# Kernel optimization log

Hardware: AMD Instinct MI355X
Metric: run time of the kernel (lower is better)

The kernel has to match this reference:

```python
import jax, jax.numpy as jnp
import numpy as np

C = 128
HEAD_CHANNEL = 32
NUM_HEAD = C // HEAD_CHANNEL
SCALE = HEAD_CHANNEL ** 0.5
EPS = 1e-5


def _layernorm(x, g, b):
    mu = jnp.mean(x, axis=-1, keepdims=True)
    var = jnp.mean((x - mu) ** 2, axis=-1, keepdims=True)
    return (x - mu) * jax.lax.rsqrt(var + EPS) * g + b


def _proj(x, g, b, w1, b1, w2, b2):
    # LayerNorm -> Linear(C,2C) -> LeakyReLU(0.01) -> Linear(2C,C); dropout=0 (identity)
    h = jax.nn.leaky_relu(_layernorm(x, g, b) @ w1 + b1, negative_slope=0.01)
    return h @ w2 + b2


def _mlp(x, w1, b1, w2, b2):
    h = jax.nn.leaky_relu(x @ w1 + b1, negative_slope=0.01)
    return h @ w2 + b2


def setup_inputs() -> dict:
    key = jax.random.key(0)
    ks = jax.random.split(key, 32)
    s = 1.0 / np.sqrt(C)
    s2 = 1.0 / np.sqrt(2 * C)
    d = {}
    d["q"] = jax.random.normal(ks[0], (2, C, 64, 64), jnp.float32)
    d["k"] = jax.random.normal(ks[1], (2, C, 64, 64), jnp.float32)
    d["v"] = jax.random.normal(ks[2], (2, C, 64, 64), jnp.float32)
    i = 3
    for p in ("q", "k", "v"):
        d[f"ln_{p}_g"] = jnp.ones((C,), jnp.float32)
        d[f"ln_{p}_b"] = jnp.zeros((C,), jnp.float32)
        d[f"w{p}1"] = jax.random.uniform(ks[i], (C, 2 * C), jnp.float32, -s, s); i += 1
        d[f"b{p}1"] = jnp.zeros((2 * C,), jnp.float32)
        d[f"w{p}2"] = jax.random.uniform(ks[i], (2 * C, C), jnp.float32, -s2, s2); i += 1
        d[f"b{p}2"] = jnp.zeros((C,), jnp.float32)
    for m in ("m1", "m2"):
        d[f"{m}_w1"] = jax.random.uniform(ks[i], (C, 2 * C), jnp.float32, -s, s); i += 1
        d[f"{m}_b1"] = jnp.zeros((2 * C,), jnp.float32)
        d[f"{m}_w2"] = jax.random.uniform(ks[i], (2 * C, C), jnp.float32, -s2, s2); i += 1
        d[f"{m}_b2"] = jnp.zeros((C,), jnp.float32)
    return d


def reference(q, k, v,
              ln_q_g, ln_q_b, wq1, bq1, wq2, bq2,
              ln_k_g, ln_k_b, wk1, bk1, wk2, bk2,
              ln_v_g, ln_v_b, wv1, bv1, wv2, bv2,
              m1_w1, m1_b1, m1_w2, m1_b2,
              m2_w1, m2_b1, m2_w2, m2_b2):
    B, Cc, H, W = q.shape
    S = H * W
    # [B,C,H,W] -> [B,S,C] token layout
    qt = q.transpose(0, 2, 3, 1).reshape(B, S, Cc)
    kt = k.transpose(0, 2, 3, 1).reshape(B, S, Cc)
    vt = v.transpose(0, 2, 3, 1).reshape(B, S, Cc)
    qp = _proj(qt, ln_q_g, ln_q_b, wq1, bq1, wq2, bq2)
    kp = _proj(kt, ln_k_g, ln_k_b, wk1, bk1, wk2, bk2)
    vp = _proj(vt, ln_v_g, ln_v_b, wv1, bv1, wv2, bv2)  # v_attn_1
    qh = qp.reshape(B, S, NUM_HEAD, HEAD_CHANNEL)
    kh = kp.reshape(B, S, NUM_HEAD, HEAD_CHANNEL)
    vh = vp.reshape(B, S, NUM_HEAD, HEAD_CHANNEL)
    attn = jax.nn.softmax(jnp.einsum('bqhd,bkhd->bhqk', qh, kh) / SCALE, axis=-1)
    x = jnp.einsum('bhqk,bkhd->bqhd', attn, vh).reshape(B, S, Cc)
    rs1 = vp + _mlp(x, m1_w1, m1_b1, m1_w2, m1_b2)
    rs2 = rs1 + _mlp(rs1, m2_w1, m2_b1, m2_w2, m2_b2)
    # back to [B,C,H,W]
    return rs2.reshape(B, H, W, Cc).transpose(0, 3, 1, 2)
```

## Files before the change

kernel.cpp:

```cpp
#include <hip/hip_runtime.h>
#include <hip/hip_bf16.h>

typedef __bf16 bf16_t;
typedef __bf16 bf16x4 __attribute__((ext_vector_type(4)));
typedef __bf16 bf16x8 __attribute__((ext_vector_type(8)));
typedef float f32x4 __attribute__((ext_vector_type(4)));
typedef float f32x16 __attribute__((ext_vector_type(16)));


static constexpr size_t WS_WPK   = 0;
static constexpr size_t WS_PP    = 655360;
static constexpr size_t WS_VT    = WS_PP + 3ull*2097152;
static constexpr size_t WS_OPART = WS_VT + 2097152;
static constexpr size_t WS_LPART = WS_OPART + 16777216;

struct WPtrs { const float* w1[5]; const float* w2[5]; };

__global__ __launch_bounds__(256) void prep_weights(WPtrs wp, bf16_t* __restrict__ dst) {
    __shared__ float ts[64][65];
    int bx = blockIdx.x;
    int p = bx >> 4;
    int t = bx & 15;
    const float* src; int sld, dld, r0, c0; bf16_t* d;
    if (t < 8) {
        src = wp.w1[p]; sld = 256; dld = 128;
        r0 = (t >> 2) * 64; c0 = (t & 3) * 64;
        d = dst + p * 65536;
    } else {
        int tt = t - 8;
        src = wp.w2[p]; sld = 128; dld = 256;
        r0 = (tt >> 1) * 64; c0 = (tt & 1) * 64;
        d = dst + p * 65536 + 32768;
    }
    for (int i = threadIdx.x; i < 4096; i += 256) {
        int r = i >> 6, c = i & 63;
        ts[r][c] = src[(r0 + r) * sld + c0 + c];
    }
    __syncthreads();
    for (int i = threadIdx.x; i < 4096; i += 256) {
        int c = i >> 6, r = i & 63;
        d[(c0 + c) * dld + (r0 + r)] = (bf16_t)ts[r][c];
    }
}

struct ProjArgs {
    const float* src[3]; const float* g[3]; const float* bb[3];
    const float* B1[3]; const float* B2[3];
    bf16_t* OUT[3]; bf16_t* VTOUT;
};

__global__ __launch_bounds__(256) void projln_kernel(ProjArgs a, const bf16_t* __restrict__ wpk) {
    __shared__ float xs[16][132];
    __shared__ bf16_t al[16][136];
    __shared__ bf16_t hl[16][264];
    int z = blockIdx.y;
    int m0 = blockIdx.x * 16;
    int b = m0 >> 12, s0 = m0 & 4095;
    int tx = threadIdx.x;
    int w = tx >> 6;
    int lane = tx & 63;
    int quad = lane >> 4;
    int l15 = lane & 15;

    const float* src = a.src[z];
    for (int idx = tx; idx < 2048; idx += 256) {
        int c = idx >> 4, tt = idx & 15;
        xs[tt][c] = src[(b * 128 + c) * 4096 + s0 + tt];
    }
    __syncthreads();

    {
        int t = tx >> 4, j = tx & 15;
        float sum = 0.f, sq = 0.f;
#pragma unroll
        for (int k = 0; k < 8; ++k) { float v = xs[t][j + 16 * k]; sum += v; sq += v * v; }
        sum += __shfl_xor(sum, 1); sq += __shfl_xor(sq, 1);
        sum += __shfl_xor(sum, 2); sq += __shfl_xor(sq, 2);
        sum += __shfl_xor(sum, 4); sq += __shfl_xor(sq, 4);
        sum += __shfl_xor(sum, 8); sq += __shfl_xor(sq, 8);
        float mu = sum * (1.0f / 128.0f);
        float var = sq * (1.0f / 128.0f) - mu * mu;
        float rs = rsqrtf(var + 1e-5f);
        const float* g = a.g[z];
        const float* bb = a.bb[z];
#pragma unroll
        for (int k = 0; k < 8; ++k) {
            int c = j + 16 * k;
            al[t][c] = (bf16_t)((xs[t][c] - mu) * rs * g[c] + bb[c]);
        }
    }
    __syncthreads();

    const bf16_t* w1t = wpk + (size_t)z * 65536;
    const bf16_t* w2t = w1t + 32768;
    bf16x8 af[4];
#pragma unroll
    for (int kt = 0; kt < 4; ++kt) af[kt] = *(const bf16x8*)(&al[l15][kt * 32 + quad * 8]);

#pragma unroll
    for (int sub = 0; sub < 4; ++sub) {
        int n = w * 64 + sub * 16 + l15;
        const bf16_t* wrow = w1t + (size_t)n * 128 + quad * 8;
        f32x4 acc = {0.f, 0.f, 0.f, 0.f};
#pragma unroll
        for (int kt = 0; kt < 4; ++kt) {
            bf16x8 bfrag = *(const bf16x8*)(wrow + kt * 32);
            acc = __builtin_amdgcn_mfma_f32_16x16x32_bf16(af[kt], bfrag, acc, 0, 0, 0);
        }
        float bn = a.B1[z][n];
#pragma unroll
        for (int r = 0; r < 4; ++r) {
            float v = acc[r] + bn;
            v = v > 0.f ? v : 0.01f * v;
            hl[quad * 4 + r][n] = (bf16_t)v;
        }
    }
    __syncthreads();

    bf16x8 hf[8];
#pragma unroll
    for (int kt = 0; kt < 8; ++kt)
        hf[kt] = *(const bf16x8*)(&hl[l15][kt * 32 + quad * 8]);

#pragma unroll
    for (int sub = 0; sub < 2; ++sub) {
        int n = w * 32 + sub * 16 + l15;
        const bf16_t* wrow = w2t + (size_t)n * 256 + quad * 8;
        f32x4 acc = {0.f, 0.f, 0.f, 0.f};
#pragma unroll
        for (int kt = 0; kt < 8; ++kt) {
            bf16x8 bfrag = *(const bf16x8*)(wrow + kt * 32);
            acc = __builtin_amdgcn_mfma_f32_16x16x32_bf16(hf[kt], bfrag, acc, 0, 0, 0);
        }
        float bn = a.B2[z][n];
        float vals[4];
#pragma unroll
        for (int r = 0; r < 4; ++r) vals[r] = acc[r] + bn;
#pragma unroll
        for (int r = 0; r < 4; ++r)
            a.OUT[z][(size_t)(m0 + quad * 4 + r) * 128 + n] = (bf16_t)vals[r];
        if (z == 2) {
            int bh = b * 4 + (n >> 5), d = n & 31;
            bf16x4 tv = {(bf16_t)vals[0], (bf16_t)vals[1], (bf16_t)vals[2], (bf16_t)vals[3]};
            *(bf16x4*)(a.VTOUT + ((size_t)(bh * 32 + d)) * 4096 + s0 + quad * 4) = tv;
        }
    }
}

__global__ __launch_bounds__(256, 4) void attn_kernel(const bf16_t* __restrict__ qp,
                                                      const bf16_t* __restrict__ kp,
                                                      const bf16_t* __restrict__ vt,
                                                      bf16_t* __restrict__ opart,
                                                      float* __restrict__ lpart) {
    int lid = blockIdx.x;
    int bh = lid & 7;
    int r = lid >> 3;
    int split = r & 7;
    int qb = r >> 3;
    int w = threadIdx.x >> 6;
    int lane = threadIdx.x & 63;
    int l31 = lane & 31;
    int h5 = lane >> 5;
    int b = bh >> 2, h = bh & 3;
    int q0 = qb * 256 + w * 64;

    constexpr float kScale = 0.17677669529663687f * 1.4426950408889634f;

    bf16x8 qf[2][2];
#pragma unroll
    for (int s = 0; s < 2; ++s) {
        const bf16_t* qrow = qp + ((size_t)(b * 4096 + q0 + s * 32 + l31)) * 128 + h * 32 + h5 * 8;
        bf16x8 q0r = *(const bf16x8*)(qrow);
        bf16x8 q1r = *(const bf16x8*)(qrow + 16);
#pragma unroll
        for (int j = 0; j < 8; ++j) {
            qf[s][0][j] = (bf16_t)((float)q0r[j] * kScale);
            qf[s][1][j] = (bf16_t)((float)q1r[j] * kScale);
        }
    }

    bf16x8 a_up, a_lo;
    {
        bf16_t one = (bf16_t)1.0f, zer = (bf16_t)0.0f;
#pragma unroll
        for (int j = 0; j < 8; ++j) { a_up[j] = (l31 < 16) ? one : zer; a_lo[j] = (l31 < 16) ? zer : one; }
    }

    int key_m = (l31 & ~12) | ((l31 & 4) << 1) | ((l31 & 8) >> 1);
    const bf16_t* kbase = kp + ((size_t)(b * 4096) + key_m) * 128 + h * 32 + h5 * 8;
    const bf16_t* vbase = vt + ((size_t)(bh * 32) + l31) * 4096 + h5 * 8;

    f32x16 acca = {0.f,0.f,0.f,0.f,0.f,0.f,0.f,0.f,0.f,0.f,0.f,0.f,0.f,0.f,0.f,0.f};
    f32x16 accb = acca, lacc = acca;
    f32x16 zero16 = acca;

    int kt0 = split * 16;
    const bf16_t* kpt = kbase + (size_t)kt0 * 4096;
    const bf16_t* vpt = vbase + kt0 * 32;
    bf16x8 kf0 = *(const bf16x8*)(kpt);
    bf16x8 kf1 = *(const bf16x8*)(kpt + 16);
    bf16x8 vf0 = *(const bf16x8*)(vpt);
    bf16x8 vf1 = *(const bf16x8*)(vpt + 16);

    for (int it = 0; it < 16; ++it) {
        const bf16_t* nkpt = kpt + (it < 15 ? 4096 : 0);
        const bf16_t* nvpt = vpt + (it < 15 ? 32 : 0);
        bf16x8 nk0 = *(const bf16x8*)(nkpt);
        bf16x8 nk1 = *(const bf16x8*)(nkpt + 16);
        bf16x8 nv0 = *(const bf16x8*)(nvpt);
        bf16x8 nv1 = *(const bf16x8*)(nvpt + 16);

        f32x16 sca = __builtin_amdgcn_mfma_f32_32x32x16_bf16(kf0, qf[0][0], zero16, 0, 0, 0);
        sca = __builtin_amdgcn_mfma_f32_32x32x16_bf16(kf1, qf[0][1], sca, 0, 0, 0);
        f32x16 scb = __builtin_amdgcn_mfma_f32_32x32x16_bf16(kf0, qf[1][0], zero16, 0, 0, 0);
        scb = __builtin_amdgcn_mfma_f32_32x32x16_bf16(kf1, qf[1][1], scb, 0, 0, 0);

        bf16x8 pfa0, pfa1, pfb0, pfb1;
#pragma unroll
        for (int j = 0; j < 8; ++j) {
            pfa0[j] = (bf16_t)__builtin_amdgcn_exp2f(sca[j]);
            pfa1[j] = (bf16_t)__builtin_amdgcn_exp2f(sca[8 + j]);
            pfb0[j] = (bf16_t)__builtin_amdgcn_exp2f(scb[j]);
            pfb1[j] = (bf16_t)__builtin_amdgcn_exp2f(scb[8 + j]);
        }

        lacc = __builtin_amdgcn_mfma_f32_32x32x16_bf16(a_up, pfa0, lacc, 0, 0, 0);
        lacc = __builtin_amdgcn_mfma_f32_32x32x16_bf16(a_up, pfa1, lacc, 0, 0, 0);
        lacc = __builtin_amdgcn_mfma_f32_32x32x16_bf16(a_lo, pfb0, lacc, 0, 0, 0);
        lacc = __builtin_amdgcn_mfma_f32_32x32x16_bf16(a_lo, pfb1, lacc, 0, 0, 0);

        acca = __builtin_amdgcn_mfma_f32_32x32x16_bf16(vf0, pfa0, acca, 0, 0, 0);
        acca = __builtin_amdgcn_mfma_f32_32x32x16_bf16(vf1, pfa1, acca, 0, 0, 0);
        accb = __builtin_amdgcn_mfma_f32_32x32x16_bf16(vf0, pfb0, accb, 0, 0, 0);
        accb = __builtin_amdgcn_mfma_f32_32x32x16_bf16(vf1, pfb1, accb, 0, 0, 0);

        kf0 = nk0; kf1 = nk1; vf0 = nv0; vf1 = nv1;
        kpt = nkpt; vpt = nvpt;
    }

    size_t obase0 = ((size_t)(bh * 8 + split) * 4096 + q0 + l31) * 32;
#pragma unroll
    for (int g = 0; g < 4; ++g) {
        bf16x4 ov = {(bf16_t)acca[4*g], (bf16_t)acca[4*g+1], (bf16_t)acca[4*g+2], (bf16_t)acca[4*g+3]};
        *(bf16x4*)(opart + obase0 + 8 * g + 4 * h5) = ov;
    }
    size_t obase1 = obase0 + 32ull * 32;
#pragma unroll
    for (int g = 0; g < 4; ++g) {
        bf16x4 ov = {(bf16_t)accb[4*g], (bf16_t)accb[4*g+1], (bf16_t)accb[4*g+2], (bf16_t)accb[4*g+3]};
        *(bf16x4*)(opart + obase1 + 8 * g + 4 * h5) = ov;
    }
    lpart[(bh * 8 + split) * 4096 + q0 + h5 * 32 + l31] = h5 ? lacc[8] : lacc[0];
}

__global__ __launch_bounds__(256) void mlpf_kernel(const bf16_t* __restrict__ opart,
                                                   const float* __restrict__ lpart,
                                                   const bf16_t* __restrict__ wpk,
                                                   const float* __restrict__ b1a,
                                                   const float* __restrict__ b2a,
                                                   const float* __restrict__ b1b,
                                                   const float* __restrict__ b2b,
                                                   const bf16_t* __restrict__ vp,
                                                   float* __restrict__ out) {
    __shared__ bf16_t al[16][136];
    __shared__ bf16_t al2[16][136];
    __shared__ bf16_t hl[16][264];
    int w = threadIdx.x >> 6;
    int lane = threadIdx.x & 63;
    int quad = lane >> 4;
    int l15 = lane & 15;
    int m0 = blockIdx.x * 16;
    int bb = m0 >> 12, s0 = m0 & 4095;

    const bf16_t* w1ta = wpk + 3ull * 65536;
    const bf16_t* w2ta = w1ta + 32768;
    const bf16_t* w1tb = wpk + 4ull * 65536;
    const bf16_t* w2tb = w1tb + 32768;

    {
        int t = threadIdx.x >> 4;
        int cg = threadIdx.x & 15;
        int m = m0 + t;
        int qq = m & 4095;
        int h = cg >> 2, d0 = (cg & 3) * 8;
        int bh = bb * 4 + h;
        float accv[8] = {0.f, 0.f, 0.f, 0.f, 0.f, 0.f, 0.f, 0.f};
        float l = 0.f;
#pragma unroll
        for (int s = 0; s < 8; ++s) {
            const bf16_t* op = opart + ((size_t)((bh * 8 + s) * 4096) + qq) * 32 + d0;
            bf16x8 o8 = *(const bf16x8*)op;
#pragma unroll
            for (int j = 0; j < 8; ++j) accv[j] += (float)o8[j];
            l += lpart[(bh * 8 + s) * 4096 + qq];
        }
        float invl = 1.0f / l;
        bf16x8 a8;
#pragma unroll
        for (int j = 0; j < 8; ++j) a8[j] = (bf16_t)(accv[j] * invl);
        *(bf16x8*)(&al[t][cg * 8]) = a8;
    }
    __syncthreads();

    bf16x8 af[4];
#pragma unroll
    for (int kt = 0; kt < 4; ++kt) af[kt] = *(const bf16x8*)(&al[l15][kt * 32 + quad * 8]);
#pragma unroll
    for (int sub = 0; sub < 4; ++sub) {
        int n = w * 64 + sub * 16 + l15;
        const bf16_t* wrow = w1ta + (size_t)n * 128 + quad * 8;
        f32x4 acc = {0.f, 0.f, 0.f, 0.f};
#pragma unroll
        for (int kt = 0; kt < 4; ++kt) {
            bf16x8 bfrag = *(const bf16x8*)(wrow + kt * 32);
            acc = __builtin_amdgcn_mfma_f32_16x16x32_bf16(af[kt], bfrag, acc, 0, 0, 0);
        }
        float bn = b1a[n];
#pragma unroll
        for (int r = 0; r < 4; ++r) {
            float v = acc[r] + bn;
            v = v > 0.f ? v : 0.01f * v;
            hl[quad * 4 + r][n] = (bf16_t)v;
        }
    }
    __syncthreads();

    {
        bf16x8 hf[8];
#pragma unroll
        for (int kt = 0; kt < 8; ++kt)
            hf[kt] = *(const bf16x8*)(&hl[l15][kt * 32 + quad * 8]);
#pragma unroll
        for (int sub = 0; sub < 2; ++sub) {
            int n = w * 32 + sub * 16 + l15;
            const bf16_t* wrow = w2ta + (size_t)n * 256 + quad * 8;
            f32x4 acc = {0.f, 0.f, 0.f, 0.f};
#pragma unroll
            for (int kt = 0; kt < 8; ++kt) {
                bf16x8 bfrag = *(const bf16x8*)(wrow + kt * 32);
                acc = __builtin_amdgcn_mfma_f32_16x16x32_bf16(hf[kt], bfrag, acc, 0, 0, 0);
            }
            float bn = b2a[n];
#pragma unroll
            for (int r = 0; r < 4; ++r) {
                int m = m0 + quad * 4 + r;
                float v = acc[r] + bn + (float)vp[(size_t)m * 128 + n];
                al2[quad * 4 + r][n] = (bf16_t)v;
            }
        }
    }
    __syncthreads();

    bf16x8 af2[4];
#pragma unroll
    for (int kt = 0; kt < 4; ++kt) af2[kt] = *(const bf16x8*)(&al2[l15][kt * 32 + quad * 8]);
#pragma unroll
    for (int sub = 0; sub < 4; ++sub) {
        int n = w * 64 + sub * 16 + l15;
        const bf16_t* wrow = w1tb + (size_t)n * 128 + quad * 8;
        f32x4 acc = {0.f, 0.f, 0.f, 0.f};
#pragma unroll
        for (int kt = 0; kt < 4; ++kt) {
            bf16x8 bfrag = *(const bf16x8*)(wrow + kt * 32);
            acc = __builtin_amdgcn_mfma_f32_16x16x32_bf16(af2[kt], bfrag, acc, 0, 0, 0);
        }
        float bn = b1b[n];
#pragma unroll
        for (int r = 0; r < 4; ++r) {
            float v = acc[r] + bn;
            v = v > 0.f ? v : 0.01f * v;
            hl[quad * 4 + r][n] = (bf16_t)v;
        }
    }
    __syncthreads();

    {
        bf16x8 hf[8];
#pragma unroll
        for (int kt = 0; kt < 8; ++kt)
            hf[kt] = *(const bf16x8*)(&hl[l15][kt * 32 + quad * 8]);
#pragma unroll
        for (int sub = 0; sub < 2; ++sub) {
            int n = w * 32 + sub * 16 + l15;
            const bf16_t* wrow = w2tb + (size_t)n * 256 + quad * 8;
            f32x4 acc = {0.f, 0.f, 0.f, 0.f};
#pragma unroll
            for (int kt = 0; kt < 8; ++kt) {
                bf16x8 bfrag = *(const bf16x8*)(wrow + kt * 32);
                acc = __builtin_amdgcn_mfma_f32_16x16x32_bf16(hf[kt], bfrag, acc, 0, 0, 0);
            }
            float bn = b2b[n];
            f32x4 ov;
#pragma unroll
            for (int r = 0; r < 4; ++r)
                ov[r] = acc[r] + bn + (float)al2[quad * 4 + r][n];
            *(f32x4*)(out + ((size_t)(bb * 128 + n)) * 4096 + s0 + quad * 4) = ov;
        }
    }
}

extern "C" void kernel_launch(void* const* d_in, const int* in_sizes, int n_in,
                              void* d_out, int out_size, void* d_ws, size_t ws_size,
                              hipStream_t stream) {
    const float* q = (const float*)d_in[0];
    const float* k = (const float*)d_in[1];
    const float* v = (const float*)d_in[2];
    const float* ln_g[3] = {(const float*)d_in[3], (const float*)d_in[9], (const float*)d_in[15]};
    const float* ln_b[3] = {(const float*)d_in[4], (const float*)d_in[10], (const float*)d_in[16]};
    const float* w1[5] = {(const float*)d_in[5], (const float*)d_in[11], (const float*)d_in[17],
                          (const float*)d_in[21], (const float*)d_in[25]};
    const float* b1[5] = {(const float*)d_in[6], (const float*)d_in[12], (const float*)d_in[18],
                          (const float*)d_in[22], (const float*)d_in[26]};
    const float* w2[5] = {(const float*)d_in[7], (const float*)d_in[13], (const float*)d_in[19],
                          (const float*)d_in[23], (const float*)d_in[27]};
    const float* b2[5] = {(const float*)d_in[8], (const float*)d_in[14], (const float*)d_in[20],
                          (const float*)d_in[24], (const float*)d_in[28]};
    float* out = (float*)d_out;

    char* ws = (char*)d_ws;
    bf16_t* wpk = (bf16_t*)(ws + WS_WPK);
    bf16_t* pp  = (bf16_t*)(ws + WS_PP);
    bf16_t* vtb = (bf16_t*)(ws + WS_VT);
    bf16_t* opart = (bf16_t*)(ws + WS_OPART);
    float* lpart = (float*)(ws + WS_LPART);

    WPtrs wp;
    for (int p = 0; p < 5; ++p) { wp.w1[p] = w1[p]; wp.w2[p] = w2[p]; }
    prep_weights<<<80, 256, 0, stream>>>(wp, wpk);

    ProjArgs pa;
    pa.src[0] = q; pa.src[1] = k; pa.src[2] = v;
    for (int i = 0; i < 3; ++i) {
        pa.g[i] = ln_g[i]; pa.bb[i] = ln_b[i];
        pa.B1[i] = b1[i]; pa.B2[i] = b2[i];
        pa.OUT[i] = pp + (size_t)i * 1048576;
    }
    pa.VTOUT = vtb;
    projln_kernel<<<dim3(512, 3), 256, 0, stream>>>(pa, wpk);

    attn_kernel<<<1024, 256, 0, stream>>>(pp, pp + 1048576, vtb, opart, lpart);

    mlpf_kernel<<<512, 256, 0, stream>>>(opart, lpart, wpk,
                                         b1[3], b2[3], b1[4], b2[4],
                                         pp + 2ull * 1048576, out);
}
```

Baseline: 207.5 us.

## Halve attention key splits and software-pipeline QK with PV across iterations

Reduces the key-dimension split from 8 to 4, so each attention block handles 32 key tiles and the grid shrinks to 512 blocks. This halves the partial-output buffer and the reduction work in the MLP kernel. The loop is restructured so the next tile's QK^T MFMAs are issued after the current tile's exp and PV MFMAs, overlapping the exp latency with matrix work. Launch bounds are relaxed to 2 blocks per SIMD to allow more registers, at the cost of occupancy and fewer blocks to fill the GPU.

```diff
diff --git a/kernel.cpp b/kernel.cpp
--- a/kernel.cpp
+++ b/kernel.cpp
@@ -12,7 +12,7 @@
 static constexpr size_t WS_PP    = 655360;
 static constexpr size_t WS_VT    = WS_PP + 3ull*2097152;
 static constexpr size_t WS_OPART = WS_VT + 2097152;
-static constexpr size_t WS_LPART = WS_OPART + 16777216;
+static constexpr size_t WS_LPART = WS_OPART + 8388608;
 
 struct WPtrs { const float* w1[5]; const float* w2[5]; };
 
@@ -147,7 +147,7 @@
     }
 }
 
-__global__ __launch_bounds__(256, 4) void attn_kernel(const bf16_t* __restrict__ qp,
+__global__ __launch_bounds__(256, 2) void attn_kernel(const bf16_t* __restrict__ qp,
                                                       const bf16_t* __restrict__ kp,
                                                       const bf16_t* __restrict__ vt,
                                                       bf16_t* __restrict__ opart,
@@ -155,8 +155,8 @@
     int lid = blockIdx.x;
     int bh = lid & 7;
     int r = lid >> 3;
-    int split = r & 7;
-    int qb = r >> 3;
+    int split = r & 3;
+    int qb = r >> 2;
     int w = threadIdx.x >> 6;
     int lane = threadIdx.x & 63;
     int l31 = lane & 31;
@@ -187,33 +187,34 @@
     }
 
     int key_m = (l31 & ~12) | ((l31 & 4) << 1) | ((l31 & 8) >> 1);
-    const bf16_t* kbase = kp + ((size_t)(b * 4096) + key_m) * 128 + h * 32 + h5 * 8;
-    const bf16_t* vbase = vt + ((size_t)(bh * 32) + l31) * 4096 + h5 * 8;
+    const bf16_t* kbase = kp + ((size_t)(b * 4096) + split * 1024 + key_m) * 128 + h * 32 + h5 * 8;
+    const bf16_t* vbase = vt + ((size_t)(bh * 32) + l31) * 4096 + split * 1024 + h5 * 8;
 
     f32x16 acca = {0.f,0.f,0.f,0.f,0.f,0.f,0.f,0.f,0.f,0.f,0.f,0.f,0.f,0.f,0.f,0.f};
     f32x16 accb = acca, lacc = acca;
     f32x16 zero16 = acca;
 
-    int kt0 = split * 16;
-    const bf16_t* kpt = kbase + (size_t)kt0 * 4096;
-    const bf16_t* vpt = vbase + kt0 * 32;
-    bf16x8 kf0 = *(const bf16x8*)(kpt);
-    bf16x8 kf1 = *(const bf16x8*)(kpt + 16);
-    bf16x8 vf0 = *(const bf16x8*)(vpt);
-    bf16x8 vf1 = *(const bf16x8*)(vpt + 16);
-
-    for (int it = 0; it < 16; ++it) {
-        const bf16_t* nkpt = kpt + (it < 15 ? 4096 : 0);
-        const bf16_t* nvpt = vpt + (it < 15 ? 32 : 0);
-        bf16x8 nk0 = *(const bf16x8*)(nkpt);
-        bf16x8 nk1 = *(const bf16x8*)(nkpt + 16);
-        bf16x8 nv0 = *(const bf16x8*)(nvpt);
-        bf16x8 nv1 = *(const bf16x8*)(nvpt + 16);
-
-        f32x16 sca = __builtin_amdgcn_mfma_f32_32x32x16_bf16(kf0, qf[0][0], zero16, 0, 0, 0);
-        sca = __builtin_amdgcn_mfma_f32_32x32x16_bf16(kf1, qf[0][1], sca, 0, 0, 0);
-        f32x16 scb = __builtin_amdgcn_mfma_f32_32x32x16_bf16(kf0, qf[1][0], zero16, 0, 0, 0);
-        scb = __builtin_amdgcn_mfma_f32_32x32x16_bf16(kf1, qf[1][1], scb, 0, 0, 0);
+    bf16x8 kcur0 = *(const bf16x8*)(kbase);
+    bf16x8 kcur1 = *(const bf16x8*)(kbase + 16);
+    bf16x8 vuse0 = *(const bf16x8*)(vbase);
+    bf16x8 vuse1 = *(const bf16x8*)(vbase + 16);
+
+    f32x16 sca = __builtin_amdgcn_mfma_f32_32x32x16_bf16(kcur0, qf[0][0], zero16, 0, 0, 0);
+    sca = __builtin_amdgcn_mfma_f32_32x32x16_bf16(kcur1, qf[0][1], sca, 0, 0, 0);
+    f32x16 scb = __builtin_amdgcn_mfma_f32_32x32x16_bf16(kcur0, qf[1][0], zero16, 0, 0, 0);
+    scb = __builtin_amdgcn_mfma_f32_32x32x16_bf16(kcur1, qf[1][1], scb, 0, 0, 0);
+
+    bf16x8 kfB0 = *(const bf16x8*)(kbase + 4096);
+    bf16x8 kfB1 = *(const bf16x8*)(kbase + 4096 + 16);
+    bf16x8 vfB0 = *(const bf16x8*)(vbase + 32);
+    bf16x8 vfB1 = *(const bf16x8*)(vbase + 32 + 16);
+
+    for (int it = 1; it < 32; ++it) {
+        int nt = (it < 31) ? it + 1 : 31;
+        bf16x8 nk0 = *(const bf16x8*)(kbase + (size_t)nt * 4096);
+        bf16x8 nk1 = *(const bf16x8*)(kbase + (size_t)nt * 4096 + 16);
+        bf16x8 nv0 = *(const bf16x8*)(vbase + nt * 32);
+        bf16x8 nv1 = *(const bf16x8*)(vbase + nt * 32 + 16);
 
         bf16x8 pfa0, pfa1, pfb0, pfb1;
 #pragma unroll
@@ -223,22 +224,44 @@
             pfb0[j] = (bf16_t)__builtin_amdgcn_exp2f(scb[j]);
             pfb1[j] = (bf16_t)__builtin_amdgcn_exp2f(scb[8 + j]);
         }
-
         lacc = __builtin_amdgcn_mfma_f32_32x32x16_bf16(a_up, pfa0, lacc, 0, 0, 0);
         lacc = __builtin_amdgcn_mfma_f32_32x32x16_bf16(a_up, pfa1, lacc, 0, 0, 0);
         lacc = __builtin_amdgcn_mfma_f32_32x32x16_bf16(a_lo, pfb0, lacc, 0, 0, 0);
         lacc = __builtin_amdgcn_mfma_f32_32x32x16_bf16(a_lo, pfb1, lacc, 0, 0, 0);
-
-        acca = __builtin_amdgcn_mfma_f32_32x32x16_bf16(vf0, pfa0, acca, 0, 0, 0);
-        acca = __builtin_amdgcn_mfma_f32_32x32x16_bf16(vf1, pfa1, acca, 0, 0, 0);
-        accb = __builtin_amdgcn_mfma_f32_32x32x16_bf16(vf0, pfb0, accb, 0, 0, 0);
-        accb = __builtin_amdgcn_mfma_f32_32x32x16_bf16(vf1, pfb1, accb, 0, 0, 0);
-
-        kf0 = nk0; kf1 = nk1; vf0 = nv0; vf1 = nv1;
-        kpt = nkpt; vpt = nvpt;
-    }
-
-    size_t obase0 = ((size_t)(bh * 8 + split) * 4096 + q0 + l31) * 32;
+        acca = __builtin_amdgcn_mfma_f32_32x32x16_bf16(vuse0, pfa0, acca, 0, 0, 0);
+        acca = __builtin_amdgcn_mfma_f32_32x32x16_bf16(vuse1, pfa1, acca, 0, 0, 0);
+        accb = __builtin_amdgcn_mfma_f32_32x32x16_bf16(vuse0, pfb0, accb, 0, 0, 0);
+        accb = __builtin_amdgcn_mfma_f32_32x32x16_bf16(vuse1, pfb1, accb, 0, 0, 0);
+
+        sca = __builtin_amdgcn_mfma_f32_32x32x16_bf16(kfB0, qf[0][0], zero16, 0, 0, 0);
+        sca = __builtin_amdgcn_mfma_f32_32x32x16_bf16(kfB1, qf[0][1], sca, 0, 0, 0);
+        scb = __builtin_amdgcn_mfma_f32_32x32x16_bf16(kfB0, qf[1][0], zero16, 0, 0, 0);
+        scb = __builtin_amdgcn_mfma_f32_32x32x16_bf16(kfB1, qf[1][1], scb, 0, 0, 0);
+
+        vuse0 = vfB0; vuse1 = vfB1;
+        kfB0 = nk0; kfB1 = nk1; vfB0 = nv0; vfB1 = nv1;
+    }
+
+    {
+        bf16x8 pfa0, pfa1, pfb0, pfb1;
+#pragma unroll
+        for (int j = 0; j < 8; ++j) {
+            pfa0[j] = (bf16_t)__builtin_amdgcn_exp2f(sca[j]);
+            pfa1[j] = (bf16_t)__builtin_amdgcn_exp2f(sca[8 + j]);
+            pfb0[j] = (bf16_t)__builtin_amdgcn_exp2f(scb[j]);
+            pfb1[j] = (bf16_t)__builtin_amdgcn_exp2f(scb[8 + j]);
+        }
+        lacc = __builtin_amdgcn_mfma_f32_32x32x16_bf16(a_up, pfa0, lacc, 0, 0, 0);
+        lacc = __builtin_amdgcn_mfma_f32_32x32x16_bf16(a_up, pfa1, lacc, 0, 0, 0);
+        lacc = __builtin_amdgcn_mfma_f32_32x32x16_bf16(a_lo, pfb0, lacc, 0, 0, 0);
+        lacc = __builtin_amdgcn_mfma_f32_32x32x16_bf16(a_lo, pfb1, lacc, 0, 0, 0);
+        acca = __builtin_amdgcn_mfma_f32_32x32x16_bf16(vuse0, pfa0, acca, 0, 0, 0);
+        acca = __builtin_amdgcn_mfma_f32_32x32x16_bf16(vuse1, pfa1, acca, 0, 0, 0);
+        accb = __builtin_amdgcn_mfma_f32_32x32x16_bf16(vuse0, pfb0, accb, 0, 0, 0);
+        accb = __builtin_amdgcn_mfma_f32_32x32x16_bf16(vuse1, pfb1, accb, 0, 0, 0);
+    }
+
+    size_t obase0 = ((size_t)(bh * 4 + split) * 4096 + q0 + l31) * 32;
 #pragma unroll
     for (int g = 0; g < 4; ++g) {
         bf16x4 ov = {(bf16_t)acca[4*g], (bf16_t)acca[4*g+1], (bf16_t)acca[4*g+2], (bf16_t)acca[4*g+3]};
@@ -250,7 +273,7 @@
         bf16x4 ov = {(bf16_t)accb[4*g], (bf16_t)accb[4*g+1], (bf16_t)accb[4*g+2], (bf16_t)accb[4*g+3]};
         *(bf16x4*)(opart + obase1 + 8 * g + 4 * h5) = ov;
     }
-    lpart[(bh * 8 + split) * 4096 + q0 + h5 * 32 + l31] = h5 ? lacc[8] : lacc[0];
+    lpart[(bh * 4 + split) * 4096 + q0 + h5 * 32 + l31] = h5 ? lacc[8] : lacc[0];
 }
 
 __global__ __launch_bounds__(256) void mlpf_kernel(const bf16_t* __restrict__ opart,
@@ -287,12 +310,12 @@
         float accv[8] = {0.f, 0.f, 0.f, 0.f, 0.f, 0.f, 0.f, 0.f};
         float l = 0.f;
 #pragma unroll
-        for (int s = 0; s < 8; ++s) {
-            const bf16_t* op = opart + ((size_t)((bh * 8 + s) * 4096) + qq) * 32 + d0;
+        for (int s = 0; s < 4; ++s) {
+            const bf16_t* op = opart + ((size_t)((bh * 4 + s) * 4096) + qq) * 32 + d0;
             bf16x8 o8 = *(const bf16x8*)op;
 #pragma unroll
             for (int j = 0; j < 8; ++j) accv[j] += (float)o8[j];
-            l += lpart[(bh * 8 + s) * 4096 + qq];
+            l += lpart[(bh * 4 + s) * 4096 + qq];
         }
         float invl = 1.0f / l;
         bf16x8 a8;
@@ -438,7 +461,7 @@
     pa.VTOUT = vtb;
     projln_kernel<<<dim3(512, 3), 256, 0, stream>>>(pa, wpk);
 
-    attn_kernel<<<1024, 256, 0, stream>>>(pp, pp + 1048576, vtb, opart, lpart);
+    attn_kernel<<<512, 256, 0, stream>>>(pp, pp + 1048576, vtb, opart, lpart);
 
     mlpf_kernel<<<512, 256, 0, stream>>>(opart, lpart, wpk,
                                          b1[3], b2[3], b1[4], b2[4],
```

Result: faster. 201.6 us (-2.8%).

## Fuse attention with both MLPs, reducing key-split partials in shared memory

Applied to the files above, without the earlier changes.

Merges the attention kernel and the MLP kernel into one launch. Each 512-thread block owns 32 query tokens across all 4 heads, with the key range split in two halves across waves. The partial outputs and row sums are combined in LDS rather than written to and re-read from global opart/lpart buffers. This removes the global partial round trip and one launch, and software-pipelines the QK^T MFMA one tile ahead of the PV step. The trade-off is a grid of only 256 blocks, each doing a 64-iteration serial key loop, which may under-fill the GPU compared with the previous 1024-block, 8-way key split.

```diff
diff --git a/kernel.cpp b/kernel.cpp
--- a/kernel.cpp
+++ b/kernel.cpp
@@ -8,11 +8,9 @@
 typedef float f32x16 __attribute__((ext_vector_type(16)));
 
 
-static constexpr size_t WS_WPK   = 0;
-static constexpr size_t WS_PP    = 655360;
-static constexpr size_t WS_VT    = WS_PP + 3ull*2097152;
-static constexpr size_t WS_OPART = WS_VT + 2097152;
-static constexpr size_t WS_LPART = WS_OPART + 16777216;
+static constexpr size_t WS_WPK = 0;
+static constexpr size_t WS_PP  = 655360;
+static constexpr size_t WS_VT  = WS_PP + 3ull*2097152;
 
 struct WPtrs { const float* w1[5]; const float* w2[5]; };
 
@@ -147,254 +145,255 @@
     }
 }
 
-__global__ __launch_bounds__(256, 4) void attn_kernel(const bf16_t* __restrict__ qp,
-                                                      const bf16_t* __restrict__ kp,
-                                                      const bf16_t* __restrict__ vt,
-                                                      bf16_t* __restrict__ opart,
-                                                      float* __restrict__ lpart) {
-    int lid = blockIdx.x;
-    int bh = lid & 7;
-    int r = lid >> 3;
-    int split = r & 7;
-    int qb = r >> 3;
-    int w = threadIdx.x >> 6;
-    int lane = threadIdx.x & 63;
+__global__ __launch_bounds__(512, 2) void attn_mlp_kernel(const bf16_t* __restrict__ qp,
+                                                          const bf16_t* __restrict__ kp,
+                                                          const bf16_t* __restrict__ vt,
+                                                          const bf16_t* __restrict__ vp,
+                                                          const bf16_t* __restrict__ wpk,
+                                                          const float* __restrict__ b1a,
+                                                          const float* __restrict__ b2a,
+                                                          const float* __restrict__ b1b,
+                                                          const float* __restrict__ b2b,
+                                                          float* __restrict__ out) {
+    __shared__ bf16_t opl[2][32][136];
+    __shared__ float ll[2][4][32];
+    __shared__ bf16_t xl[32][136];
+    __shared__ bf16_t al2[32][136];
+    __shared__ bf16_t hl[32][264];
+
+    int tx = threadIdx.x;
+    int wid = tx >> 6;
+    int h = wid & 3;
+    int half = wid >> 2;
+    int lane = tx & 63;
     int l31 = lane & 31;
     int h5 = lane >> 5;
-    int b = bh >> 2, h = bh & 3;
-    int q0 = qb * 256 + w * 64;
+    int quad = lane >> 4;
+    int l15 = lane & 15;
+    int wq = lane >> 4;
+    (void)wq;
+
+    int t0 = blockIdx.x * 32;
+    int b = t0 >> 12;
+    int s0 = t0 & 4095;
+    int bh = b * 4 + h;
 
     constexpr float kScale = 0.17677669529663687f * 1.4426950408889634f;
 
-    bf16x8 qf[2][2];
-#pragma unroll
-    for (int s = 0; s < 2; ++s) {
-        const bf16_t* qrow = qp + ((size_t)(b * 4096 + q0 + s * 32 + l31)) * 128 + h * 32 + h5 * 8;
-        bf16x8 q0r = *(const bf16x8*)(qrow);
-        bf16x8 q1r = *(const bf16x8*)(qrow + 16);
+    const bf16_t* qrow = qp + ((size_t)(b * 4096 + s0 + l31)) * 128 + h * 32 + h5 * 8;
+    bf16x8 q0r = *(const bf16x8*)(qrow);
+    bf16x8 q1r = *(const bf16x8*)(qrow + 16);
+    bf16x8 qf0, qf1;
+#pragma unroll
+    for (int j = 0; j < 8; ++j) {
+        qf0[j] = (bf16_t)((float)q0r[j] * kScale);
+        qf1[j] = (bf16_t)((float)q1r[j] * kScale);
+    }
+
+    bf16x8 a_ones;
+#pragma unroll
+    for (int j = 0; j < 8; ++j) a_ones[j] = (bf16_t)1.0f;
+
+    int key_m = (l31 & ~12) | ((l31 & 4) << 1) | ((l31 & 8) >> 1);
+    const bf16_t* kb = kp + ((size_t)(b * 4096) + half * 2048 + key_m) * 128 + h * 32 + h5 * 8;
+    const bf16_t* vb = vt + ((size_t)(bh * 32) + l31) * 4096 + half * 2048 + h5 * 8;
+
+    f32x16 acca = {0.f,0.f,0.f,0.f,0.f,0.f,0.f,0.f,0.f,0.f,0.f,0.f,0.f,0.f,0.f,0.f};
+    f32x16 lacc = acca;
+    f32x16 zero16 = acca;
+
+    bf16x8 kcur0 = *(const bf16x8*)(kb);
+    bf16x8 kcur1 = *(const bf16x8*)(kb + 16);
+    bf16x8 vuse0 = *(const bf16x8*)(vb);
+    bf16x8 vuse1 = *(const bf16x8*)(vb + 16);
+
+    f32x16 sca = __builtin_amdgcn_mfma_f32_32x32x16_bf16(kcur0, qf0, zero16, 0, 0, 0);
+    sca = __builtin_amdgcn_mfma_f32_32x32x16_bf16(kcur1, qf1, sca, 0, 0, 0);
+
+    bf16x8 kfB0 = *(const bf16x8*)(kb + 4096);
+    bf16x8 kfB1 = *(const bf16x8*)(kb + 4096 + 16);
+    bf16x8 vfB0 = *(const bf16x8*)(vb + 32);
+    bf16x8 vfB1 = *(const bf16x8*)(vb + 32 + 16);
+
+    for (int it = 1; it < 64; ++it) {
+        int nt = (it < 63) ? it + 1 : 63;
+        bf16x8 nk0 = *(const bf16x8*)(kb + (size_t)nt * 4096);
+        bf16x8 nk1 = *(const bf16x8*)(kb + (size_t)nt * 4096 + 16);
+        bf16x8 nv0 = *(const bf16x8*)(vb + nt * 32);
+        bf16x8 nv1 = *(const bf16x8*)(vb + nt * 32 + 16);
+
+        bf16x8 pf0, pf1;
 #pragma unroll
         for (int j = 0; j < 8; ++j) {
-            qf[s][0][j] = (bf16_t)((float)q0r[j] * kScale);
-            qf[s][1][j] = (bf16_t)((float)q1r[j] * kScale);
-        }
-    }
-
-    bf16x8 a_up, a_lo;
-    {
-        bf16_t one = (bf16_t)1.0f, zer = (bf16_t)0.0f;
-#pragma unroll
-        for (int j = 0; j < 8; ++j) { a_up[j] = (l31 < 16) ? one : zer; a_lo[j] = (l31 < 16) ? zer : one; }
-    }
-
-    int key_m = (l31 & ~12) | ((l31 & 4) << 1) | ((l31 & 8) >> 1);
-    const bf16_t* kbase = kp + ((size_t)(b * 4096) + key_m) * 128 + h * 32 + h5 * 8;
-    const bf16_t* vbase = vt + ((size_t)(bh * 32) + l31) * 4096 + h5 * 8;
-
-    f32x16 acca = {0.f,0.f,0.f,0.f,0.f,0.f,0.f,0.f,0.f,0.f,0.f,0.f,0.f,0.f,0.f,0.f};
-    f32x16 accb = acca, lacc = acca;
-    f32x16 zero16 = acca;
-
-    int kt0 = split * 16;
-    const bf16_t* kpt = kbase + (size_t)kt0 * 4096;
-    const bf16_t* vpt = vbase + kt0 * 32;
-    bf16x8 kf0 = *(const bf16x8*)(kpt);
-    bf16x8 kf1 = *(const bf16x8*)(kpt + 16);
-    bf16x8 vf0 = *(const bf16x8*)(vpt);
-    bf16x8 vf1 = *(const bf16x8*)(vpt + 16);
-
-    for (int it = 0; it < 16; ++it) {
-        const bf16_t* nkpt = kpt + (it < 15 ? 4096 : 0);
-        const bf16_t* nvpt = vpt + (it < 15 ? 32 : 0);
-        bf16x8 nk0 = *(const bf16x8*)(nkpt);
-        bf16x8 nk1 = *(const bf16x8*)(nkpt + 16);
-        bf16x8 nv0 = *(const bf16x8*)(nvpt);
-        bf16x8 nv1 = *(const bf16x8*)(nvpt + 16);
-
-        f32x16 sca = __builtin_amdgcn_mfma_f32_32x32x16_bf16(kf0, qf[0][0], zero16, 0, 0, 0);
-        sca = __builtin_amdgcn_mfma_f32_32x32x16_bf16(kf1, qf[0][1], sca, 0, 0, 0);
-        f32x16 scb = __builtin_amdgcn_mfma_f32_32x32x16_bf16(kf0, qf[1][0], zero16, 0, 0, 0);
-        scb = __builtin_amdgcn_mfma_f32_32x32x16_bf16(kf1, qf[1][1], scb, 0, 0, 0);
-
-        bf16x8 pfa0, pfa1, pfb0, pfb1;
+            pf0[j] = (bf16_t)__builtin_amdgcn_exp2f(sca[j]);
+            pf1[j] = (bf16_t)__builtin_amdgcn_exp2f(sca[8 + j]);
+        }
+        lacc = __builtin_amdgcn_mfma_f32_32x32x16_bf16(a_ones, pf0, lacc, 0, 0, 0);
+        lacc = __builtin_amdgcn_mfma_f32_32x32x16_bf16(a_ones, pf1, lacc, 0, 0, 0);
+        acca = __builtin_amdgcn_mfma_f32_32x32x16_bf16(vuse0, pf0, acca, 0, 0, 0);
+        acca = __builtin_amdgcn_mfma_f32_32x32x16_bf16(vuse1, pf1, acca, 0, 0, 0);
+
+        sca = __builtin_amdgcn_mfma_f32_32x32x16_bf16(kfB0, qf0, zero16, 0, 0, 0);
+        sca = __builtin_amdgcn_mfma_f32_32x32x16_bf16(kfB1, qf1, sca, 0, 0, 0);
+
+        vuse0 = vfB0; vuse1 = vfB1;
+        kfB0 = nk0; kfB1 = nk1; vfB0 = nv0; vfB1 = nv1;
+    }
+    {
+        bf16x8 pf0, pf1;
 #pragma unroll
         for (int j = 0; j < 8; ++j) {
-            pfa0[j] = (bf16_t)__builtin_amdgcn_exp2f(sca[j]);
-            pfa1[j] = (bf16_t)__builtin_amdgcn_exp2f(sca[8 + j]);
-            pfb0[j] = (bf16_t)__builtin_amdgcn_exp2f(scb[j]);
-            pfb1[j] = (bf16_t)__builtin_amdgcn_exp2f(scb[8 + j]);
-        }
-
-        lacc = __builtin_amdgcn_mfma_f32_32x32x16_bf16(a_up, pfa0, lacc, 0, 0, 0);
-        lacc = __builtin_amdgcn_mfma_f32_32x32x16_bf16(a_up, pfa1, lacc, 0, 0, 0);
-        lacc = __builtin_amdgcn_mfma_f32_32x32x16_bf16(a_lo, pfb0, lacc, 0, 0, 0);
-        lacc = __builtin_amdgcn_mfma_f32_32x32x16_bf16(a_lo, pfb1, lacc, 0, 0, 0);
-
-        acca = __builtin_amdgcn_mfma_f32_32x32x16_bf16(vf0, pfa0, acca, 0, 0, 0);
-        acca = __builtin_amdgcn_mfma_f32_32x32x16_bf16(vf1, pfa1, acca, 0, 0, 0);
-        accb = __builtin_amdgcn_mfma_f32_32x32x16_bf16(vf0, pfb0, accb, 0, 0, 0);
-        accb = __builtin_amdgcn_mfma_f32_32x32x16_bf16(vf1, pfb1, accb, 0, 0, 0);
-
-        kf0 = nk0; kf1 = nk1; vf0 = nv0; vf1 = nv1;
-        kpt = nkpt; vpt = nvpt;
-    }
-
-    size_t obase0 = ((size_t)(bh * 8 + split) * 4096 + q0 + l31) * 32;
+            pf0[j] = (bf16_t)__builtin_amdgcn_exp2f(sca[j]);
+            pf1[j] = (bf16_t)__builtin_amdgcn_exp2f(sca[8 + j]);
+        }
+        lacc = __builtin_amdgcn_mfma_f32_32x32x16_bf16(a_ones, pf0, lacc, 0, 0, 0);
+        lacc = __builtin_amdgcn_mfma_f32_32x32x16_bf16(a_ones, pf1, lacc, 0, 0, 0);
+        acca = __builtin_amdgcn_mfma_f32_32x32x16_bf16(vuse0, pf0, acca, 0, 0, 0);
+        acca = __builtin_amdgcn_mfma_f32_32x32x16_bf16(vuse1, pf1, acca, 0, 0, 0);
+    }
+
 #pragma unroll
     for (int g = 0; g < 4; ++g) {
         bf16x4 ov = {(bf16_t)acca[4*g], (bf16_t)acca[4*g+1], (bf16_t)acca[4*g+2], (bf16_t)acca[4*g+3]};
-        *(bf16x4*)(opart + obase0 + 8 * g + 4 * h5) = ov;
-    }
-    size_t obase1 = obase0 + 32ull * 32;
-#pragma unroll
-    for (int g = 0; g < 4; ++g) {
-        bf16x4 ov = {(bf16_t)accb[4*g], (bf16_t)accb[4*g+1], (bf16_t)accb[4*g+2], (bf16_t)accb[4*g+3]};
-        *(bf16x4*)(opart + obase1 + 8 * g + 4 * h5) = ov;
-    }
-    lpart[(bh * 8 + split) * 4096 + q0 + h5 * 32 + l31] = h5 ? lacc[8] : lacc[0];
-}
-
-__global__ __launch_bounds__(256) void mlpf_kernel(const bf16_t* __restrict__ opart,
-                                                   const float* __restrict__ lpart,
-                                                   const bf16_t* __restrict__ wpk,
-                                                   const float* __restrict__ b1a,
-                                                   const float* __restrict__ b2a,
-                                                   const float* __restrict__ b1b,
-                                                   const float* __restrict__ b2b,
-                                                   const bf16_t* __restrict__ vp,
-                                                   float* __restrict__ out) {
-    __shared__ bf16_t al[16][136];
-    __shared__ bf16_t al2[16][136];
-    __shared__ bf16_t hl[16][264];
-    int w = threadIdx.x >> 6;
-    int lane = threadIdx.x & 63;
-    int quad = lane >> 4;
-    int l15 = lane & 15;
-    int m0 = blockIdx.x * 16;
-    int bb = m0 >> 12, s0 = m0 & 4095;
+        *(bf16x4*)(&opl[half][l31][h * 32 + 8 * g + 4 * h5]) = ov;
+    }
+    if (h5 == 0) ll[half][h][l31] = lacc[0];
+    __syncthreads();
+
+    {
+        int t = tx >> 4;
+        int cg = tx & 15;
+        int hh = cg >> 2;
+        float invl = 1.0f / (ll[0][hh][t] + ll[1][hh][t]);
+        bf16x8 o0 = *(const bf16x8*)(&opl[0][t][cg * 8]);
+        bf16x8 o1 = *(const bf16x8*)(&opl[1][t][cg * 8]);
+        bf16x8 x8;
+#pragma unroll
+        for (int j = 0; j < 8; ++j) x8[j] = (bf16_t)(((float)o0[j] + (float)o1[j]) * invl);
+        *(bf16x8*)(&xl[t][cg * 8]) = x8;
+    }
+    __syncthreads();
 
     const bf16_t* w1ta = wpk + 3ull * 65536;
     const bf16_t* w2ta = w1ta + 32768;
     const bf16_t* w1tb = wpk + 4ull * 65536;
     const bf16_t* w2tb = w1tb + 32768;
-
-    {
-        int t = threadIdx.x >> 4;
-        int cg = threadIdx.x & 15;
-        int m = m0 + t;
-        int qq = m & 4095;
-        int h = cg >> 2, d0 = (cg & 3) * 8;
-        int bh = bb * 4 + h;
-        float accv[8] = {0.f, 0.f, 0.f, 0.f, 0.f, 0.f, 0.f, 0.f};
-        float l = 0.f;
-#pragma unroll
-        for (int s = 0; s < 8; ++s) {
-            const bf16_t* op = opart + ((size_t)((bh * 8 + s) * 4096) + qq) * 32 + d0;
-            bf16x8 o8 = *(const bf16x8*)op;
-#pragma unroll
-            for (int j = 0; j < 8; ++j) accv[j] += (float)o8[j];
-            l += lpart[(bh * 8 + s) * 4096 + qq];
-        }
-        float invl = 1.0f / l;
-        bf16x8 a8;
-#pragma unroll
-        for (int j = 0; j < 8; ++j) a8[j] = (bf16_t)(accv[j] * invl);
-        *(bf16x8*)(&al[t][cg * 8]) = a8;
-    }
-    __syncthreads();
-
-    bf16x8 af[4];
-#pragma unroll
-    for (int kt = 0; kt < 4; ++kt) af[kt] = *(const bf16x8*)(&al[l15][kt * 32 + quad * 8]);
-#pragma unroll
-    for (int sub = 0; sub < 4; ++sub) {
-        int n = w * 64 + sub * 16 + l15;
-        const bf16_t* wrow = w1ta + (size_t)n * 128 + quad * 8;
-        f32x4 acc = {0.f, 0.f, 0.f, 0.f};
-#pragma unroll
-        for (int kt = 0; kt < 4; ++kt) {
+    int w8 = wid;
+
+    {
+        bf16x8 af[2][4];
+#pragma unroll
+        for (int mt = 0; mt < 2; ++mt)
+#pragma unroll
+            for (int kt = 0; kt < 4; ++kt)
+                af[mt][kt] = *(const bf16x8*)(&xl[mt * 16 + l15][kt * 32 + quad * 8]);
+#pragma unroll
+        for (int sub = 0; sub < 2; ++sub) {
+            int n = w8 * 32 + sub * 16 + l15;
+            const bf16_t* wrow = w1ta + (size_t)n * 128 + quad * 8;
+            f32x4 acc[2] = {{0.f,0.f,0.f,0.f},{0.f,0.f,0.f,0.f}};
+#pragma unroll
+            for (int kt = 0; kt < 4; ++kt) {
+                bf16x8 bfrag = *(const bf16x8*)(wrow + kt * 32);
+                acc[0] = __builtin_amdgcn_mfma_f32_16x16x32_bf16(af[0][kt], bfrag, acc[0], 0, 0, 0);
+                acc[1] = __builtin_amdgcn_mfma_f32_16x16x32_bf16(af[1][kt], bfrag, acc[1], 0, 0, 0);
+            }
+            float bn = b1a[n];
+#pragma unroll
+            for (int mt = 0; mt < 2; ++mt)
+#pragma unroll
+                for (int r = 0; r < 4; ++r) {
+                    float v = acc[mt][r] + bn;
+                    v = v > 0.f ? v : 0.01f * v;
+                    hl[mt * 16 + quad * 4 + r][n] = (bf16_t)v;
+                }
+        }
+    }
+    __syncthreads();
+
+    {
+        bf16x8 hf[2][8];
+#pragma unroll
+        for (int mt = 0; mt < 2; ++mt)
+#pragma unroll
+            for (int kt = 0; kt < 8; ++kt)
+                hf[mt][kt] = *(const bf16x8*)(&hl[mt * 16 + l15][kt * 32 + quad * 8]);
+        int n = w8 * 16 + l15;
+        const bf16_t* wrow = w2ta + (size_t)n * 256 + quad * 8;
+        f32x4 acc[2] = {{0.f,0.f,0.f,0.f},{0.f,0.f,0.f,0.f}};
+#pragma unroll
+        for (int kt = 0; kt < 8; ++kt) {
             bf16x8 bfrag = *(const bf16x8*)(wrow + kt * 32);
-            acc = __builtin_amdgcn_mfma_f32_16x16x32_bf16(af[kt], bfrag, acc, 0, 0, 0);
-        }
-        float bn = b1a[n];
-#pragma unroll
-        for (int r = 0; r < 4; ++r) {
-            float v = acc[r] + bn;
-            v = v > 0.f ? v : 0.01f * v;
-            hl[quad * 4 + r][n] = (bf16_t)v;
-        }
-    }
-    __syncthreads();
-
-    {
-        bf16x8 hf[8];
-#pragma unroll
-        for (int kt = 0; kt < 8; ++kt)
-            hf[kt] = *(const bf16x8*)(&hl[l15][kt * 32 + quad * 8]);
+            acc[0] = __builtin_amdgcn_mfma_f32_16x16x32_bf16(hf[0][kt], bfrag, acc[0], 0, 0, 0);
+            acc[1] = __builtin_amdgcn_mfma_f32_16x16x32_bf16(hf[1][kt], bfrag, acc[1], 0, 0, 0);
+        }
+        float bn = b2a[n];
+#pragma unroll
+        for (int mt = 0; mt < 2; ++mt)
+#pragma unroll
+            for (int r = 0; r < 4; ++r) {
+                int m = t0 + mt * 16 + quad * 4 + r;
+                float v = acc[mt][r] + bn + (float)vp[(size_t)m * 128 + n];
+                al2[mt * 16 + quad * 4 + r][n] = (bf16_t)v;
+            }
+    }
+    __syncthreads();
+
+    {
+        bf16x8 af[2][4];
+#pragma unroll
+        for (int mt = 0; mt < 2; ++mt)
+#pragma unroll
+            for (int kt = 0; kt < 4; ++kt)
+                af[mt][kt] = *(const bf16x8*)(&al2[mt * 16 + l15][kt * 32 + quad * 8]);
 #pragma unroll
         for (int sub = 0; sub < 2; ++sub) {
-            int n = w * 32 + sub * 16 + l15;
-            const bf16_t* wrow = w2ta + (size_t)n * 256 + quad * 8;
-            f32x4 acc = {0.f, 0.f, 0.f, 0.f};
-#pragma unroll
-            for (int kt = 0; kt < 8; ++kt) {
+            int n = w8 * 32 + sub * 16 + l15;
+            const bf16_t* wrow = w1tb + (size_t)n * 128 + quad * 8;
+            f32x4 acc[2] = {{0.f,0.f,0.f,0.f},{0.f,0.f,0.f,0.f}};
+#pragma unroll
+            for (int kt = 0; kt < 4; ++kt) {
                 bf16x8 bfrag = *(const bf16x8*)(wrow + kt * 32);
-                acc = __builtin_amdgcn_mfma_f32_16x16x32_bf16(hf[kt], bfrag, acc, 0, 0, 0);
+                acc[0] = __builtin_amdgcn_mfma_f32_16x16x32_bf16(af[0][kt], bfrag, acc[0], 0, 0, 0);
+                acc[1] = __builtin_amdgcn_mfma_f32_16x16x32_bf16(af[1][kt], bfrag, acc[1], 0, 0, 0);
             }
-            float bn = b2a[n];
-#pragma unroll
-            for (int r = 0; r < 4; ++r) {
-                int m = m0 + quad * 4 + r;
-                float v = acc[r] + bn + (float)vp[(size_t)m * 128 + n];
-                al2[quad * 4 + r][n] = (bf16_t)v;
-            }
-        }
-    }
-    __syncthreads();
-
-    bf16x8 af2[4];
-#pragma unroll
-    for (int kt = 0; kt < 4; ++kt) af2[kt] = *(const bf16x8*)(&al2[l15][kt * 32 + quad * 8]);
-#pragma unroll
-    for (int sub = 0; sub < 4; ++sub) {
-        int n = w * 64 + sub * 16 + l15;
-        const bf16_t* wrow = w1tb + (size_t)n * 128 + quad * 8;
-        f32x4 acc = {0.f, 0.f, 0.f, 0.f};
-#pragma unroll
-        for (int kt = 0; kt < 4; ++kt) {
+            float bn = b1b[n];
+#pragma unroll
+            for (int mt = 0; mt < 2; ++mt)
+#pragma unroll
+                for (int r = 0; r < 4; ++r) {
+                    float v = acc[mt][r] + bn;
+                    v = v > 0.f ? v : 0.01f * v;
+                    hl[mt * 16 + quad * 4 + r][n] = (bf16_t)v;
+                }
+        }
+    }
+    __syncthreads();
+
+    {
+        bf16x8 hf[2][8];
+#pragma unroll
+        for (int mt = 0; mt < 2; ++mt)
+#pragma unroll
+            for (int kt = 0; kt < 8; ++kt)
+                hf[mt][kt] = *(const bf16x8*)(&hl[mt * 16 + l15][kt * 32 + quad * 8]);
+        int n = w8 * 16 + l15;
+        const bf16_t* wrow = w2tb + (size_t)n * 256 + quad * 8;
+        f32x4 acc[2] = {{0.f,0.f,0.f,0.f},{0.f,0.f,0.f,0.f}};
+#pragma unroll
+        for (int kt = 0; kt < 8; ++kt) {
             bf16x8 bfrag = *(const bf16x8*)(wrow + kt * 32);
-            acc = __builtin_amdgcn_mfma_f32_16x16x32_bf16(af2[kt], bfrag, acc, 0, 0, 0);
-        }
-        float bn = b1b[n];
-#pragma unroll
-        for (int r = 0; r < 4; ++r) {
-            float v = acc[r] + bn;
-            v = v > 0.f ? v : 0.01f * v;
-            hl[quad * 4 + r][n] = (bf16_t)v;
-        }
-    }
-    __syncthreads();
-
-    {
-        bf16x8 hf[8];
-#pragma unroll
-        for (int kt = 0; kt < 8; ++kt)
-            hf[kt] = *(const bf16x8*)(&hl[l15][kt * 32 + quad * 8]);
-#pragma unroll
-        for (int sub = 0; sub < 2; ++sub) {
-            int n = w * 32 + sub * 16 + l15;
-            const bf16_t* wrow = w2tb + (size_t)n * 256 + quad * 8;
-            f32x4 acc = {0.f, 0.f, 0.f, 0.f};
-#pragma unroll
-            for (int kt = 0; kt < 8; ++kt) {
-                bf16x8 bfrag = *(const bf16x8*)(wrow + kt * 32);
-                acc = __builtin_amdgcn_mfma_f32_16x16x32_bf16(hf[kt], bfrag, acc, 0, 0, 0);
-            }
-            float bn = b2b[n];
+            acc[0] = __builtin_amdgcn_mfma_f32_16x16x32_bf16(hf[0][kt], bfrag, acc[0], 0, 0, 0);
+            acc[1] = __builtin_amdgcn_mfma_f32_16x16x32_bf16(hf[1][kt], bfrag, acc[1], 0, 0, 0);
+        }
+        float bn = b2b[n];
+#pragma unroll
+        for (int mt = 0; mt < 2; ++mt) {
             f32x4 ov;
 #pragma unroll
             for (int r = 0; r < 4; ++r)
-                ov[r] = acc[r] + bn + (float)al2[quad * 4 + r][n];
-            *(f32x4*)(out + ((size_t)(bb * 128 + n)) * 4096 + s0 + quad * 4) = ov;
+                ov[r] = acc[mt][r] + bn + (float)al2[mt * 16 + quad * 4 + r][n];
+            *(f32x4*)(out + ((size_t)(b * 128 + n)) * 4096 + s0 + mt * 16 + quad * 4) = ov;
         }
     }
 }
@@ -421,8 +420,6 @@
     bf16_t* wpk = (bf16_t*)(ws + WS_WPK);
     bf16_t* pp  = (bf16_t*)(ws + WS_PP);
     bf16_t* vtb = (bf16_t*)(ws + WS_VT);
-    bf16_t* opart = (bf16_t*)(ws + WS_OPART);
-    float* lpart = (float*)(ws + WS_LPART);
 
     WPtrs wp;
     for (int p = 0; p < 5; ++p) { wp.w1[p] = w1[p]; wp.w2[p] = w2[p]; }
@@ -438,9 +435,7 @@
     pa.VTOUT = vtb;
     projln_kernel<<<dim3(512, 3), 256, 0, stream>>>(pa, wpk);
 
-    attn_kernel<<<1024, 256, 0, stream>>>(pp, pp + 1048576, vtb, opart, lpart);
-
-    mlpf_kernel<<<512, 256, 0, stream>>>(opart, lpart, wpk,
-                                         b1[3], b2[3], b1[4], b2[4],
-                                         pp + 2ull * 1048576, out);
+    attn_mlp_kernel<<<256, 512, 0, stream>>>(pp, pp + 1048576, vtb,
+                                             pp + 2ull * 1048576, wpk,
+                                             b1[3], b2[3], b1[4], b2[4], out);
 }
```

Result: slower. 216.5 us (+4.3%).
